# Performance work log

Measured on AMD Instinct MI355X. Metric: run time of the kernel, lower is better.

Reference implementation:

```python
import jax, jax.numpy as jnp
import numpy as np

C_IN, CH, HCH, NFFT, HOP, NL, K = 100, 512, 1536, 1024, 256, 8, 4
B, T = 16, 1024

def conv1d(x, w, b=None, pad=0, groups=1):
    # x: [B, Cin, L], w: [Cout, Cin/groups, K]
    y = jax.lax.conv_general_dilated(x, w, (1,), [(pad, pad)],
        dimension_numbers=('NCH', 'OIH', 'NCH'), feature_group_count=groups)
    if b is not None:
        y = y + b[None, :, None]
    return y

def layernorm(x, g, b, eps=1e-5):
    # normalize over last axis (channel), torch LayerNorm semantics (biased var)
    mu = jnp.mean(x, -1, keepdims=True)
    var = jnp.var(x, -1, keepdims=True)
    return (x - mu) * jax.lax.rsqrt(var + eps) * g + b

def setup_inputs() -> dict:
    key = jax.random.key(0)
    ks = jax.random.split(key, 8)
    r = lambda k, s: jax.random.normal(k, s, jnp.float32) * 0.02
    return {
        'x': jax.random.normal(ks[0], (B, C_IN, T), jnp.float32),
        'in_w': r(ks[1], (CH, C_IN, 7)), 'in_b': jnp.zeros((CH,), jnp.float32),
        'norm_g': jnp.ones((CH,), jnp.float32), 'norm_b': jnp.zeros((CH,), jnp.float32),
        'dw_w': r(ks[2], (NL, CH, 1, 7)), 'dw_b': jnp.zeros((NL, CH), jnp.float32),
        'ln_g': jnp.ones((NL, CH), jnp.float32), 'ln_b': jnp.zeros((NL, CH), jnp.float32),
        'pw1_w': r(ks[3], (NL, HCH, CH)), 'pw1_b': jnp.zeros((NL, HCH), jnp.float32),
        'pw2_w': r(ks[4], (NL, CH, HCH)), 'pw2_b': jnp.zeros((NL, CH), jnp.float32),
        'ls': jnp.full((NL, CH), 1.0 / NL, jnp.float32),
        'normL_g': jnp.ones((CH,), jnp.float32), 'normL_b': jnp.zeros((CH,), jnp.float32),
        'out_w': r(ks[5], (NFFT, CH, 1)), 'out_b': jnp.zeros((NFFT,), jnp.float32),
        'ov_w': r(ks[6], (HOP, NFFT, K)),
    }

def reference(x, in_w, in_b, norm_g, norm_b, dw_w, dw_b, ln_g, ln_b,
              pw1_w, pw1_b, pw2_w, pw2_b, ls, normL_g, normL_b, out_w, out_b, ov_w):
    x = conv1d(x, in_w, in_b, pad=3)                                   # [B, CH, T]
    x = layernorm(x.transpose(0, 2, 1), norm_g, norm_b).transpose(0, 2, 1)

    def layer(h, p):
        dw, db, g, b, w1, b1, w2, b2, s = p
        y = conv1d(h, dw, db, pad=3, groups=CH)                        # depthwise 7-tap
        y = layernorm(y.transpose(0, 2, 1), g, b)                      # [B, T, CH]
        y = jnp.einsum('btc,hc->bth', y, w1) + b1                      # pointwise expand
        y = jax.nn.gelu(y, approximate=False)
        y = jnp.einsum('bth,ch->btc', y, w2) + b2                      # pointwise project
        return h + (y * s).transpose(0, 2, 1), None

    x, _ = jax.lax.scan(layer, x, (dw_w, dw_b, ln_g, ln_b, pw1_w, pw1_b, pw2_w, pw2_b, ls))
    x = layernorm(x.transpose(0, 2, 1), normL_g, normL_b).transpose(0, 2, 1)
    o = conv1d(x, out_w, out_b, pad=0)                                 # [B, NFFT, T]
    # --- overlap_add ---
    o = conv1d(o, ov_w, None, pad=K - 1)                               # [B, HOP, L], L = T + K - 1
    Bn, C, L = o.shape
    pad_size = C * K - L + K - 1
    o = jnp.pad(o, ((0, 0), (0, 0), (0, pad_size)))
    idx = (jnp.arange(L)[None, :] + jnp.arange(C)[:, None] * (C * K - 1)) % L  # [C, L]
    o = jnp.take_along_axis(o, jnp.broadcast_to(idx[None], (Bn, C, L)), axis=2)
    o = jnp.sum(o, axis=1, keepdims=True)                              # [B, 1, L]
    return o[..., K // 2 : L - K // 2 + 1]                             # [B, 1, T]
```

## Files before the change

### kernel.cpp

```cpp
#include <hip/hip_runtime.h>

#define B_    16
#define CIN   100
#define T_    1024
#define CH_   512
#define HCH_  1536
#define NL_   8
#define NFFT_ 1024
#define HOP_  256
#define BT    (B_ * T_)
#define L_    1027
#define OROWS 1032
#define KIN   704

typedef __bf16 bf16x8 __attribute__((ext_vector_type(8)));
typedef float f32x4 __attribute__((ext_vector_type(4)));
typedef short s16x8 __attribute__((ext_vector_type(8)));
typedef short s16x4 __attribute__((ext_vector_type(4)));

__device__ __forceinline__ short f2b(float f) {
  unsigned u = __float_as_uint(f);
  u += 0x7fffu + ((u >> 16) & 1u);
  return (short)(u >> 16);
}
__device__ __forceinline__ float b2f(short s) {
  return __uint_as_float(((unsigned)(unsigned short)s) << 16);
}

__device__ __forceinline__ float fast_gelu(float x) {
  float ax = fabsf(x);
  float z = 0.7978845608f * ax * (1.f + 0.044715f * ax * ax);
  float e = __expf(-2.f * z);
  float th = 1.f - 2.f * e * __builtin_amdgcn_rcpf(1.f + e);
  float g = copysignf(th, x);
  return 0.5f * x * (1.f + g);
}

__device__ __forceinline__ void gl2lds16(const void* g, void* l) {
  __builtin_amdgcn_global_load_lds(
      (__attribute__((address_space(1))) void*)g,
      (__attribute__((address_space(3))) void*)l, 16, 0, 0);
}

__global__ __launch_bounds__(256) void k_cvt4(const float* __restrict__ s,
                                              short* __restrict__ d, int n4) {
  for (int i = blockIdx.x * 256 + threadIdx.x; i < n4; i += gridDim.x * 256) {
    f32x4 v = *reinterpret_cast<const f32x4*>(&s[i * 4]);
    s16x4 o = {f2b(v[0]), f2b(v[1]), f2b(v[2]), f2b(v[3])};
    *reinterpret_cast<s16x4*>(&d[i * 4]) = o;
  }
}

__global__ __launch_bounds__(256) void k_cvt_ov(const float* __restrict__ w,
                                                short* __restrict__ d) {
  const int n = HOP_ * NFFT_;
  for (int i = blockIdx.x * 256 + threadIdx.x; i < n; i += gridDim.x * 256) {
    f32x4 v = *reinterpret_cast<const f32x4*>(&w[(size_t)i * 4]);
#pragma unroll
    for (int k = 0; k < 4; ++k) d[(size_t)k * n + i] = f2b(v[k]);
  }
}

__global__ __launch_bounds__(256) void k_cvt_inw(const float* __restrict__ w,
                                                 short* __restrict__ d) {
  const int n = CH_ * KIN;
  for (int i = blockIdx.x * 256 + threadIdx.x; i < n; i += gridDim.x * 256) {
    int c = i / KIN, e = i - c * KIN;
    d[i] = (e < 700) ? f2b(w[c * 700 + e]) : (short)0;
  }
}

__global__ __launch_bounds__(256) void k_cvt_dwt(const float* __restrict__ w,
                                                 float* __restrict__ d) {
  const int n = NL_ * 7 * CH_;
  for (int i = blockIdx.x * 256 + threadIdx.x; i < n; i += gridDim.x * 256) {
    int l = i / (7 * CH_), r = i - l * 7 * CH_;
    int k = r >> 9, c = r & 511;
    d[i] = w[((size_t)l * CH_ + c) * 7 + k];
  }
}

__global__ __launch_bounds__(256) void k_im2col(const float* __restrict__ x,
                                                short* __restrict__ xim) {
  const int total = BT * KIN;
  for (int i = blockIdx.x * 256 + threadIdx.x; i < total; i += gridDim.x * 256) {
    int m = i / KIN, e = i - m * KIN;
    int b = m >> 10, t = m & 1023;
    int ci = e / 7, k = e - ci * 7;
    int tt = t + k - 3;
    float v = (e < 700 && tt >= 0 && tt < T_) ? x[((b * CIN + ci) << 10) + tt] : 0.f;
    xim[i] = f2b(v);
  }
}

__global__ __launch_bounds__(256) void k_zeropad(short* __restrict__ o1p) {
  int i = blockIdx.x * 256 + threadIdx.x;
  int b = i >> 13;
  int r8 = (i >> 10) & 7;
  int nn = i & 1023;
  int row = r8 < 4 ? r8 : (OROWS - 8 + r8);
  o1p[((size_t)b * OROWS + row) * NFFT_ + nn] = 0;
}

__global__ __launch_bounds__(256) void k_lnb(const short* __restrict__ in,
                                             short* __restrict__ outp,
                                             const float* __restrict__ g,
                                             const float* __restrict__ bta) {
  int row = blockIdx.x, tid = threadIdx.x;
  unsigned u = *reinterpret_cast<const unsigned*>(&in[(size_t)row * CH_ + tid * 2]);
  float v0 = __uint_as_float(u << 16);
  float v1 = __uint_as_float(u & 0xffff0000u);
  float s = v0 + v1, q = v0 * v0 + v1 * v1;
#pragma unroll
  for (int o = 32; o > 0; o >>= 1) { s += __shfl_down(s, o); q += __shfl_down(q, o); }
  __shared__ float sh[8];
  int wid = tid >> 6, lane = tid & 63;
  if (lane == 0) { sh[wid] = s; sh[wid + 4] = q; }
  __syncthreads();
  float S = sh[0] + sh[1] + sh[2] + sh[3];
  float Q = sh[4] + sh[5] + sh[6] + sh[7];
  float mu  = S * (1.f / 512.f);
  float var = Q * (1.f / 512.f) - mu * mu;
  float r = rsqrtf(var + 1e-5f);
  float x0 = (v0 - mu) * r * g[tid * 2]     + bta[tid * 2];
  float x1 = (v1 - mu) * r * g[tid * 2 + 1] + bta[tid * 2 + 1];
  unsigned o = ((unsigned)(unsigned short)f2b(x0)) |
               (((unsigned)(unsigned short)f2b(x1)) << 16);
  *reinterpret_cast<unsigned*>(&outp[(size_t)row * CH_ + tid * 2]) = o;
}

__global__ __launch_bounds__(256) void k_dwln(const short* __restrict__ h,
                                              const float* __restrict__ dwt,
                                              const float* __restrict__ dwb,
                                              const float* __restrict__ g,
                                              const float* __restrict__ bta,
                                              short* __restrict__ yb) {
  int b = blockIdx.x, t0 = blockIdx.y * 32;
  int tid = threadIdx.x, lane = tid & 63, w = tid >> 6;
  __shared__ short hs[38][512];
  for (int e = tid; e < 38 * 64; e += 256) {
    int row = e >> 6, seg = (e & 63) << 3;
    int t = t0 - 3 + row;
    s16x8 v = {};
    if (t >= 0 && t < T_)
      v = *reinterpret_cast<const s16x8*>(&h[((size_t)((b << 10) + t)) * CH_ + seg]);
    *reinterpret_cast<s16x8*>(&hs[row][seg]) = v;
  }
  const int c0 = lane << 3;
  float wk[7][8];
#pragma unroll
  for (int k = 0; k < 7; ++k) {
    f32x4 lo = *reinterpret_cast<const f32x4*>(&dwt[k * CH_ + c0]);
    f32x4 hi = *reinterpret_cast<const f32x4*>(&dwt[k * CH_ + c0 + 4]);
#pragma unroll
    for (int j = 0; j < 4; ++j) { wk[k][j] = lo[j]; wk[k][j + 4] = hi[j]; }
  }
  float bb[8], gg[8], be[8];
  {
    f32x4 a = *reinterpret_cast<const f32x4*>(&dwb[c0]);
    f32x4 b4 = *reinterpret_cast<const f32x4*>(&dwb[c0 + 4]);
    f32x4 c = *reinterpret_cast<const f32x4*>(&g[c0]);
    f32x4 d = *reinterpret_cast<const f32x4*>(&g[c0 + 4]);
    f32x4 e = *reinterpret_cast<const f32x4*>(&bta[c0]);
    f32x4 f = *reinterpret_cast<const f32x4*>(&bta[c0 + 4]);
#pragma unroll
    for (int j = 0; j < 4; ++j) {
      bb[j] = a[j]; bb[j + 4] = b4[j];
      gg[j] = c[j]; gg[j + 4] = d[j];
      be[j] = e[j]; be[j + 4] = f[j];
    }
  }
  __syncthreads();
#pragma unroll
  for (int i = 0; i < 8; ++i) {
    int r = w * 8 + i;
    float acc[8];
#pragma unroll
    for (int j = 0; j < 8; ++j) acc[j] = bb[j];
#pragma unroll
    for (int k = 0; k < 7; ++k) {
      s16x8 hv = *reinterpret_cast<const s16x8*>(&hs[r + k][c0]);
#pragma unroll
      for (int j = 0; j < 8; ++j) acc[j] += b2f(hv[j]) * wk[k][j];
    }
    float s = 0.f, q = 0.f;
#pragma unroll
    for (int j = 0; j < 8; ++j) { s += acc[j]; q += acc[j] * acc[j]; }
#pragma unroll
    for (int o = 32; o > 0; o >>= 1) { s += __shfl_xor(s, o); q += __shfl_xor(q, o); }
    float mu  = s * (1.f / 512.f);
    float var = q * (1.f / 512.f) - mu * mu;
    float rr = rsqrtf(var + 1e-5f);
    s16x8 ov;
#pragma unroll
    for (int j = 0; j < 8; ++j) ov[j] = f2b((acc[j] - mu) * rr * gg[j] + be[j]);
    *reinterpret_cast<s16x8*>(&yb[((size_t)((b << 10) + t0 + r)) * CH_ + c0]) = ov;
  }
}

template <int MODE, int BK>
__global__ __launch_bounds__(256) void k_mgemm(const short* __restrict__ A,
                                               const short* __restrict__ Bw,
                                               const float* __restrict__ bias,
                                               const float* __restrict__ scale,
                                               short* __restrict__ obf,
                                               int N, int K) {
  constexpr int CPR  = BK / 8;
  constexpr int NCH  = BK / 16;
  constexpr int TILE = 128 * BK;
  constexpr int SSH  = (BK == 32) ? 1 : 0;
  constexpr int SMEM = (4 * TILE > 16384) ? 4 * TILE : 16384;
  __shared__ __align__(16) short smem[SMEM];
  const int tid = threadIdx.x;
  const int lane = tid & 63, w = tid >> 6;
  const int id = blockIdx.x;
  const int ny = N >> 7;
  const int g8 = id >> 3;
  const int gq = g8 / ny;
  const int mt = (id & 7) + (gq << 3);
  const int nt_ = g8 - gq * ny;
  const int m0 = mt << 7, n0 = nt_ << 7;
  const int wr = (w >> 1) * 64, wc = (w & 1) * 64;
  f32x4 acc[4][4];
#pragma unroll
  for (int i = 0; i < 4; ++i)
#pragma unroll
    for (int j = 0; j < 4; ++j) acc[i][j] = (f32x4){0.f, 0.f, 0.f, 0.f};

  const short* Ab = A + (size_t)m0 * K;
  const short* Bb = Bw + (size_t)n0 * K;
  int r_[NCH], kk_[NCH];
#pragma unroll
  for (int j = 0; j < NCH; ++j) {
    int c = tid + j * 256;
    r_[j] = c / CPR;
    kk_[j] = (((c % CPR) ^ ((r_[j] >> SSH) & (CPR - 1))) * 8);
  }
  const int ar = wr + (lane & 15);
  const int br = wc + (lane & 15);
  const int hi = lane >> 4;
  const int nsteps = K / BK;

  auto stage = [&](int buf, int k0) {
    short* Sa = smem + buf * 2 * TILE;
    short* Sb = Sa + TILE;
#pragma unroll
    for (int j = 0; j < NCH; ++j)
      gl2lds16(Ab + (size_t)r_[j] * K + k0 + kk_[j], Sa + (j * 256 + w * 64) * 8);
#pragma unroll
    for (int j = 0; j < NCH; ++j)
      gl2lds16(Bb + (size_t)r_[j] * K + k0 + kk_[j], Sb + (j * 256 + w * 64) * 8);
  };

  stage(0, 0);
  if (nsteps > 1) stage(1, BK);
  for (int t = 0; t < nsteps; ++t) {
    const int cur = t & 1;
    if (t + 1 < nsteps) {
      if constexpr (BK == 32) asm volatile("s_waitcnt vmcnt(4)" ::: "memory");
      else                    asm volatile("s_waitcnt vmcnt(8)" ::: "memory");
    } else {
      asm volatile("s_waitcnt vmcnt(0)" ::: "memory");
    }
    __builtin_amdgcn_s_barrier();
    const short* As = smem + cur * 2 * TILE;
    const short* Bs = As + TILE;
#pragma unroll
    for (int ks = 0; ks < BK / 32; ++ks) {
      bf16x8 a[4], b[4];
#pragma unroll
      for (int f = 0; f < 4; ++f) {
        int row = ar + f * 16;
        a[f] = *reinterpret_cast<const bf16x8*>(
            &As[row * BK + (((ks * 4 + hi) ^ ((row >> SSH) & (CPR - 1))) * 8)]);
      }
#pragma unroll
      for (int f = 0; f < 4; ++f) {
        int row = br + f * 16;
        b[f] = *reinterpret_cast<const bf16x8*>(
            &Bs[row * BK + (((ks * 4 + hi) ^ ((row >> SSH) & (CPR - 1))) * 8)]);
      }
#pragma unroll
      for (int fi = 0; fi < 4; ++fi)
#pragma unroll
        for (int fj = 0; fj < 4; ++fj)
          acc[fi][fj] = __builtin_amdgcn_mfma_f32_16x16x32_bf16(a[fi], b[fj], acc[fi][fj], 0, 0, 0);
    }
    asm volatile("" ::: "memory");
    __builtin_amdgcn_s_barrier();
    if (t + 2 < nsteps) stage(cur, (t + 2) * BK);
  }
  short* Cl = smem;
  const int colbase = wc + (lane & 15);
#pragma unroll
  for (int fj = 0; fj < 4; ++fj) {
    int cl = colbase + fj * 16;
    int n = n0 + cl;
    float bi = bias[n];
    float sc = (MODE == 2) ? scale[n] : 0.f;
#pragma unroll
    for (int fi = 0; fi < 4; ++fi) {
#pragma unroll
      for (int r = 0; r < 4; ++r) {
        int rl = wr + (hi << 2) + fi * 16 + r;
        float v = acc[fi][fj][r] + bi;
        if (MODE == 1) v = fast_gelu(v);
        if (MODE == 2) v *= sc;
        Cl[rl * 128 + (cl ^ (((rl >> 2) & 3) << 4))] = f2b(v);
      }
    }
  }
  __syncthreads();
  const int cs = (lane & 15) * 8;
#pragma unroll
  for (int it = 0; it < 8; ++it) {
    int rl = w * 32 + it * 4 + (lane >> 4);
    s16x8 v = *reinterpret_cast<const s16x8*>(&Cl[rl * 128 + (cs ^ (((rl >> 2) & 3) << 4))]);
    int m = m0 + rl;
    if (MODE == 2) {
      size_t idx = (size_t)m * N + n0 + cs;
      s16x8 hv = *reinterpret_cast<const s16x8*>(&obf[idx]);
      s16x8 o;
#pragma unroll
      for (int j = 0; j < 8; ++j) o[j] = f2b(b2f(hv[j]) + b2f(v[j]));
      *reinterpret_cast<s16x8*>(&obf[idx]) = o;
    } else if (MODE == 3) {
      int bb = m >> 10, t = m & 1023;
      *reinterpret_cast<s16x8*>(&obf[((size_t)(bb * OROWS + 4 + t)) * NFFT_ + n0 + cs]) = v;
    } else {
      *reinterpret_cast<s16x8*>(&obf[(size_t)m * N + n0 + cs]) = v;
    }
  }
}

__global__ __launch_bounds__(256) void k_ovgemm(const short* __restrict__ o1p,
                                                const short* __restrict__ ovb,
                                                float* __restrict__ o2) {
  __shared__ __align__(16) short As2[2][136 * 64];
  __shared__ __align__(16) short Bs2[2][64 * 64];
  const int tid = threadIdx.x;
  const int lane = tid & 63, w = tid >> 6;
  const int id = blockIdx.x;
  const int xcd = id & 7, rr = id >> 3;
  const int ct = rr & 3, phi = rr >> 2;
  const int pp = xcd * 18 + phi;
  const int l0 = (pp % 9) * 128, c0 = ct * 64, b = pp / 9;
  const int wr = (w >> 1) * 64, wc = (w & 1) * 32;
  f32x4 acc[4][2];
#pragma unroll
  for (int i = 0; i < 4; ++i)
#pragma unroll
    for (int j = 0; j < 2; ++j) acc[i][j] = (f32x4){0.f, 0.f, 0.f, 0.f};

  const short* Ab = o1p + (size_t)b * OROWS * NFFT_;
  const int ar = wr + (lane & 15);
  const int br = wc + (lane & 15);
  const int hi = lane >> 4;
  const int sl_row = lane >> 3;
  const int sl_j   = lane & 7;
  int br_[2], bk_[2];
#pragma unroll
  for (int j = 0; j < 2; ++j) {
    int c = tid + j * 256;
    br_[j] = c >> 3;
    bk_[j] = ((c & 7) ^ (br_[j] & 7)) * 8;
  }

  auto stageA = [&](int buf, int k0) {
    for (int cg = w; cg < 17; cg += 4) {
      int lr = cg * 8 + sl_row;
      int gr = l0 + 1 + lr;
      if (gr > OROWS - 1) gr = OROWS - 1;
      int j = sl_j ^ (lr & 7);
      gl2lds16(Ab + (size_t)gr * NFFT_ + k0 + j * 8, &As2[buf][cg * 512]);
    }
  };
  auto stageB = [&](int buf, int k0, int ksh) {
    const short* Bb = ovb + ((size_t)(ksh * HOP_ + c0)) * NFFT_;
#pragma unroll
    for (int j = 0; j < 2; ++j)
      gl2lds16(Bb + (size_t)br_[j] * NFFT_ + k0 + bk_[j],
               &Bs2[buf][(j * 256 + w * 64) * 8]);
  };

  int ab = 0, bb = 0;
  stageA(0, 0);
  stageB(0, 0, 0);
  asm volatile("s_waitcnt vmcnt(0)" ::: "memory");
  __syncthreads();
  for (int t = 0; t < 64; ++t) {
    const int ksh = t & 3;
    const int nt = t + 1;
    if (nt < 64) {
      int nk0 = (nt >> 2) << 6;
      if ((nt & 3) == 0) stageA(ab ^ 1, nk0);
      stageB(bb ^ 1, nk0, nt & 3);
    }
    const short* As = As2[ab];
    const short* Bs = Bs2[bb];
#pragma unroll
    for (int ks = 0; ks < 2; ++ks) {
      bf16x8 a[4], bfr[2];
#pragma unroll
      for (int f = 0; f < 4; ++f) {
        int row = ar + f * 16 + ksh;
        a[f] = *reinterpret_cast<const bf16x8*>(&As[row * 64 + (((ks * 4 + hi) ^ (row & 7)) * 8)]);
      }
#pragma unroll
      for (int f = 0; f < 2; ++f) {
        int row = br + f * 16;
        bfr[f] = *reinterpret_cast<const bf16x8*>(&Bs[row * 64 + (((ks * 4 + hi) ^ (row & 7)) * 8)]);
      }
#pragma unroll
      for (int fi = 0; fi < 4; ++fi)
#pragma unroll
        for (int fj = 0; fj < 2; ++fj)
          acc[fi][fj] = __builtin_amdgcn_mfma_f32_16x16x32_bf16(a[fi], bfr[fj], acc[fi][fj], 0, 0, 0);
    }
    asm volatile("s_waitcnt vmcnt(0)" ::: "memory");
    __syncthreads();
    bb ^= 1;
    if (ksh == 3) ab ^= 1;
  }
  const int lb = l0 + wr + (hi << 2);
  const int cb = c0 + wc + (lane & 15);
#pragma unroll
  for (int fj = 0; fj < 2; ++fj) {
    int c = cb + fj * 16;
#pragma unroll
    for (int fi = 0; fi < 4; ++fi) {
#pragma unroll
      for (int r = 0; r < 4; ++r) {
        int l = lb + fi * 16 + r;
        if (l < L_) o2[((size_t)b * L_ + l) * HOP_ + c] = acc[fi][fj][r];
      }
    }
  }
}

__global__ __launch_bounds__(256) void k_oadd(const float* __restrict__ o2,
                                              float* __restrict__ out) {
  int b = blockIdx.x;
  int t = blockIdx.y * 256 + threadIdx.x;
  int m = t + 2;
  float s = 0.f;
  for (int c = 0; c < HOP_; ++c) {
    s += o2[((size_t)b * L_ + m) * HOP_ + c];
    m -= 4;
    if (m < 0) m += L_;
  }
  out[b * T_ + t] = s;
}

extern "C" void kernel_launch(void* const* d_in, const int* in_sizes, int n_in,
                              void* d_out, int out_size, void* d_ws, size_t ws_size,
                              hipStream_t stream) {
  const float* x      = (const float*)d_in[0];
  const float* in_w   = (const float*)d_in[1];
  const float* in_b   = (const float*)d_in[2];
  const float* norm_g = (const float*)d_in[3];
  const float* norm_b = (const float*)d_in[4];
  const float* dw_w   = (const float*)d_in[5];
  const float* dw_b   = (const float*)d_in[6];
  const float* ln_g   = (const float*)d_in[7];
  const float* ln_b   = (const float*)d_in[8];
  const float* pw1_w  = (const float*)d_in[9];
  const float* pw1_b  = (const float*)d_in[10];
  const float* pw2_w  = (const float*)d_in[11];
  const float* pw2_b  = (const float*)d_in[12];
  const float* ls     = (const float*)d_in[13];
  const float* normLg = (const float*)d_in[14];
  const float* normLb = (const float*)d_in[15];
  const float* out_w  = (const float*)d_in[16];
  const float* out_b  = (const float*)d_in[17];
  const float* ov_w   = (const float*)d_in[18];
  float* out = (float*)d_out;

  char* p = (char*)d_ws;
  short* hb   = (short*)p; p += (size_t)BT * CH_ * 2;
  short* yb   = (short*)p; p += (size_t)BT * CH_ * 2;
  short* zb   = (short*)p; p += (size_t)BT * HCH_ * 2;
  short* pw1b = (short*)p; p += (size_t)NL_ * HCH_ * CH_ * 2;
  short* pw2b = (short*)p; p += (size_t)NL_ * CH_ * HCH_ * 2;
  short* owb  = (short*)p; p += (size_t)NFFT_ * CH_ * 2;
  short* ovb  = (short*)p; p += (size_t)4 * HOP_ * NFFT_ * 2;
  float* dwt  = (float*)p; p += (size_t)NL_ * 7 * CH_ * 4;
  short* xim  = zb;
  short* wib  = zb + (size_t)BT * KIN;
  short* hbL  = yb;
  short* o1p  = zb;
  float* o2   = (float*)hb;

  k_cvt4<<<4096, 256, 0, stream>>>(pw1_w, pw1b, NL_ * HCH_ * CH_ / 4);
  k_cvt4<<<4096, 256, 0, stream>>>(pw2_w, pw2b, NL_ * CH_ * HCH_ / 4);
  k_cvt4<<<512, 256, 0, stream>>>(out_w, owb, NFFT_ * CH_ / 4);
  k_cvt_ov<<<1024, 256, 0, stream>>>(ov_w, ovb);
  k_cvt_inw<<<1408, 256, 0, stream>>>(in_w, wib);
  k_cvt_dwt<<<112, 256, 0, stream>>>(dw_w, dwt);
  k_im2col<<<8192, 256, 0, stream>>>(x, xim);

  k_mgemm<0, 64><<<512, 256, 0, stream>>>(xim, wib, in_b, nullptr, hb, CH_, KIN);
  k_lnb<<<BT, 256, 0, stream>>>(hb, hb, norm_g, norm_b);
  for (int l = 0; l < NL_; ++l) {
    k_dwln<<<dim3(B_, T_ / 32), 256, 0, stream>>>(
        hb, dwt + (size_t)l * 7 * CH_, dw_b + l * CH_,
        ln_g + l * CH_, ln_b + l * CH_, yb);
    k_mgemm<1, 32><<<1536, 256, 0, stream>>>(
        yb, pw1b + (size_t)l * HCH_ * CH_, pw1_b + l * HCH_, nullptr, zb,
        HCH_, CH_);
    k_mgemm<2, 64><<<512, 256, 0, stream>>>(
        zb, pw2b + (size_t)l * CH_ * HCH_, pw2_b + l * CH_, ls + l * CH_, hb,
        CH_, HCH_);
  }
  k_lnb<<<BT, 256, 0, stream>>>(hb, hbL, normLg, normLb);
  k_mgemm<3, 32><<<1024, 256, 0, stream>>>(hbL, owb, out_b, nullptr, o1p, NFFT_, CH_);
  k_zeropad<<<512, 256, 0, stream>>>(o1p);
  k_ovgemm<<<576, 256, 0, stream>>>(o1p, ovb, o2);
  k_oadd<<<dim3(B_, 4), 256, 0, stream>>>(o2, out);
}
```

Before: 867.7 us.

## Deepen overlap-add GEMM prefetch to two stages with counted vmcnt waits

```diff
diff --git a/kernel.cpp b/kernel.cpp
--- a/kernel.cpp
+++ b/kernel.cpp
@@ -341,8 +341,8 @@
   const int tid = threadIdx.x;
   const int lane = tid & 63, w = tid >> 6;
   const int id = blockIdx.x;
-  const int xcd = id & 7, rr = id >> 3;
-  const int ct = rr & 3, phi = rr >> 2;
+  const int xcd = id & 7, rrr = id >> 3;
+  const int ct = rrr & 3, phi = rrr >> 2;
   const int pp = xcd * 18 + phi;
   const int l0 = (pp % 9) * 128, c0 = ct * 64, b = pp / 9;
   const int wr = (w >> 1) * 64, wc = (w & 1) * 32;
@@ -383,21 +383,26 @@
                &Bs2[buf][(j * 256 + w * 64) * 8]);
   };
 
-  int ab = 0, bb = 0;
   stageA(0, 0);
   stageB(0, 0, 0);
-  asm volatile("s_waitcnt vmcnt(0)" ::: "memory");
-  __syncthreads();
+  stageB(1, 0, 1);
+  stageA(1, 64);
+
   for (int t = 0; t < 64; ++t) {
+    const int ab = (t >> 2) & 1;
+    const int bbuf = t & 1;
     const int ksh = t & 3;
-    const int nt = t + 1;
-    if (nt < 64) {
-      int nk0 = (nt >> 2) << 6;
-      if ((nt & 3) == 0) stageA(ab ^ 1, nk0);
-      stageB(bb ^ 1, nk0, nt & 3);
-    }
+    if (t == 63) {
+      asm volatile("s_waitcnt vmcnt(0)" ::: "memory");
+    } else if ((t & 3) < 2 && t < 58) {
+      if (w == 0) asm volatile("s_waitcnt vmcnt(7)" ::: "memory");
+      else        asm volatile("s_waitcnt vmcnt(6)" ::: "memory");
+    } else {
+      asm volatile("s_waitcnt vmcnt(2)" ::: "memory");
+    }
+    __builtin_amdgcn_s_barrier();
     const short* As = As2[ab];
-    const short* Bs = Bs2[bb];
+    const short* Bs = Bs2[bbuf];
 #pragma unroll
     for (int ks = 0; ks < 2; ++ks) {
       bf16x8 a[4], bfr[2];
@@ -417,10 +422,17 @@
         for (int fj = 0; fj < 2; ++fj)
           acc[fi][fj] = __builtin_amdgcn_mfma_f32_16x16x32_bf16(a[fi], bfr[fj], acc[fi][fj], 0, 0, 0);
     }
-    asm volatile("s_waitcnt vmcnt(0)" ::: "memory");
-    __syncthreads();
-    bb ^= 1;
-    if (ksh == 3) ab ^= 1;
+    asm volatile("s_waitcnt lgkmcnt(0)" ::: "memory");
+    __builtin_amdgcn_sched_barrier(0);
+    __builtin_amdgcn_s_barrier();
+    if (t + 2 < 64) {
+      int nt = t + 2;
+      stageB(bbuf, (nt >> 2) << 6, nt & 3);
+    }
+    if (ksh == 3) {
+      int nb = (t >> 2) + 2;
+      if (nb < 16) stageA(ab, nb << 6);
+    }
   }
   const int lb = l0 + wr + (hi << 2);
   const int cb = c0 + wc + (lane & 15);
```

After: 866.5 us. No clear change (-0.1%).
